# Kernel tuning notes

Hardware: AMD Instinct MI355X
Metric: run time of the kernel (lower is better)

## Reference

```python
import jax, jax.numpy as jnp
import numpy as np

N, B, HID, NPG, DEG, N_HOPS = 102400, 512, 256, 200, 32, 2
E = N * DEG
LN_EPS = 1e-5


def setup_inputs() -> dict:
    key = jax.random.key(0)
    ks = jax.random.split(key, 8)
    h = jax.random.normal(ks[0], (N, HID), jnp.float32)
    g = jax.random.normal(ks[1], (B, HID), jnp.float32)
    # sorted node->graph assignment, 200 nodes per graph
    batch = jnp.repeat(jnp.arange(B, dtype=jnp.int32), NPG)
    # intra-graph random edges: graph id per edge + local endpoints
    gid = jax.random.randint(ks[2], (E,), 0, B, jnp.int32)
    s_loc = jax.random.randint(ks[3], (E,), 0, NPG, jnp.int32)
    d_loc = jax.random.randint(ks[4], (E,), 0, NPG, jnp.int32)
    edge_index = jnp.stack([gid * NPG + s_loc, gid * NPG + d_loc])  # [2, E]
    # head MLP params: Linear(HID,2HID) -> LayerNorm(2HID) -> ReLU -> Linear(2HID,1)
    W1 = jax.random.normal(ks[5], (HID, 2 * HID), jnp.float32) * (1.0 / np.sqrt(HID))
    b1 = jnp.zeros((2 * HID,), jnp.float32)
    ln_g = jnp.ones((2 * HID,), jnp.float32)
    ln_b = jnp.zeros((2 * HID,), jnp.float32)
    W2 = jax.random.normal(ks[6], (2 * HID, 1), jnp.float32) * (1.0 / np.sqrt(2 * HID))
    b2 = jnp.zeros((1,), jnp.float32)
    return {"h": h, "g": g, "batch": batch, "edge_index": edge_index,
            "W1": W1, "b1": b1, "ln_g": ln_g, "ln_b": ln_b, "W2": W2, "b2": b2}


def reference(h, g, batch, edge_index, W1, b1, ln_g, ln_b, W2, b2):
    n = h.shape[0]
    nb = g.shape[0]
    # repeat_interleave(g, bincount(batch)) == g[batch] for sorted batch
    x = h + g[batch]                                   # [N, HID]
    z = x @ W1 + b1                                    # [N, 2*HID]
    mu = jnp.mean(z, axis=-1, keepdims=True)
    var = jnp.var(z, axis=-1, keepdims=True)           # biased, as torch LayerNorm
    z = (z - mu) * jax.lax.rsqrt(var + LN_EPS) * ln_g + ln_b
    z = jax.nn.relu(z)
    logits = (z @ W2 + b2)[:, 0]                       # [N]
    # segment softmax over each graph
    m = jax.ops.segment_max(logits, batch, num_segments=nb)
    e = jnp.exp(logits - m[batch])
    s = jax.ops.segment_sum(e, batch, num_segments=nb)
    node_prob = e / s[batch]                           # [N]
    pmax = jax.ops.segment_max(node_prob, batch, num_segments=nb)
    cand = jnp.where(node_prob >= pmax[batch], jnp.arange(n, dtype=jnp.int32), n)
    seed = jax.ops.segment_min(cand, batch, num_segments=nb)   # [B] global node ids
    # k_hop_subgraph BFS (PyG flow='source_to_target': expand target -> source)
    src, dst = edge_index[0], edge_index[1]
    nm = jnp.zeros((n,), jnp.int32).at[seed].set(1)
    for _ in range(N_HOPS):
        nm = jnp.maximum(nm, jnp.zeros((n,), jnp.int32).at[src].max(nm[dst]))
    nmb = nm > 0
    edge_mask = nmb[src] & nmb[dst]                    # [E] kept-edge mask
    edge_weight = logits[src] + logits[dst]            # [E]
    em = edge_mask.astype(jnp.int32)
    node_mask = (jnp.zeros((n,), jnp.int32).at[src].max(em).at[dst].max(em)) > 0
    return node_prob, edge_weight, edge_mask, node_mask
```

## Files before the change

### kernel.cpp

```cpp
#include <hip/hip_runtime.h>
#include <hip/hip_bf16.h>

#define HID 256
#define HID2 512
#define NPG 200
#define LN_EPS 1e-5f

typedef float f32x4 __attribute__((ext_vector_type(4)));
typedef short s16x8 __attribute__((ext_vector_type(8)));
typedef unsigned short ushort_t;

__device__ __forceinline__ ushort_t f2bf_rne(float x) {
    union { float f; unsigned int u; } c; c.f = x;
    unsigned int u = c.u;
    return (ushort_t)((u + 0x7fffu + ((u >> 16) & 1u)) >> 16);
}
__device__ __forceinline__ float bf2f(ushort_t h) {
    union { unsigned int u; float f; } c; c.u = ((unsigned int)h) << 16;
    return c.f;
}

__global__ __launch_bounds__(256)
void w1_prep_kernel(const float* __restrict__ W1,
                    ushort_t* __restrict__ w1h, ushort_t* __restrict__ w1l)
{
    const int col = blockIdx.x;
    const int k   = threadIdx.x;
    const float v = W1[(size_t)k * HID2 + col];
    const ushort_t hi = f2bf_rne(v);
    const ushort_t lo = f2bf_rne(v - bf2f(hi));
    const int tile = col >> 4, lc = col & 15;
    const int kq = k >> 5, gq = (k >> 3) & 3, j = k & 7;
    const size_t idx = ((((size_t)tile << 3) + kq) * 64 + (gq << 4) + lc) * 8 + j;
    w1h[idx] = hi;
    w1l[idx] = lo;
}

__global__ __launch_bounds__(512, 4)
void mlp_logits_mfma(const float* __restrict__ h, const float* __restrict__ g,
                     const int* __restrict__ batch,
                     const ushort_t* __restrict__ w1h, const ushort_t* __restrict__ w1l,
                     const float* __restrict__ b1,
                     const float* __restrict__ lng, const float* __restrict__ lnb,
                     const float* __restrict__ W2, const float* __restrict__ b2,
                     float* __restrict__ logits)
{
    __shared__ ushort_t xsh[64 * 256];
    __shared__ ushort_t xsl[64 * 256];
    __shared__ float prm[4 * 512];
    __shared__ float redS1[8][64];
    __shared__ float redS2[8][64];
    __shared__ float redT[8][64];
    __shared__ float muv[64], rsv[64];

    const int tid  = threadIdx.x;
    const int row0 = blockIdx.x * 64;

    {
        const int c = tid;
        prm[c]        = b1[c];
        prm[512 + c]  = lng[c];
        prm[1024 + c] = lnb[c];
        prm[1536 + c] = W2[c];
    }

    #pragma unroll
    for (int i = 0; i < 4; ++i) {
        const int ci = tid + (i << 9);
        const int r  = ci >> 5;
        const int kc = (ci & 31) << 3;
        const int grow = row0 + r;
        const int gb   = batch[grow];
        const f32x4* hp = reinterpret_cast<const f32x4*>(h + (size_t)grow * HID + kc);
        const f32x4* gp = reinterpret_cast<const f32x4*>(g + (size_t)gb   * HID + kc);
        const f32x4 h0 = __builtin_nontemporal_load(hp);
        const f32x4 h1 = __builtin_nontemporal_load(hp + 1);
        const f32x4 g0 = gp[0], g1 = gp[1];
        float xv[8] = { h0.x + g0.x, h0.y + g0.y, h0.z + g0.z, h0.w + g0.w,
                        h1.x + g1.x, h1.y + g1.y, h1.z + g1.z, h1.w + g1.w };
        ushort_t hh[8], ll[8];
        #pragma unroll
        for (int j = 0; j < 8; ++j) {
            const ushort_t hi = f2bf_rne(xv[j]);
            hh[j] = hi;
            ll[j] = f2bf_rne(xv[j] - bf2f(hi));
        }
        int byte_off = r * 512 + (kc << 1);
        byte_off ^= (r & 7) << 4;
        *reinterpret_cast<s16x8*>(reinterpret_cast<char*>(xsh) + byte_off) =
            *reinterpret_cast<const s16x8*>(hh);
        *reinterpret_cast<s16x8*>(reinterpret_cast<char*>(xsl) + byte_off) =
            *reinterpret_cast<const s16x8*>(ll);
    }
    __syncthreads();

    const int w  = tid >> 6;
    const int l  = tid & 63;
    const int lc = l & 15;
    const int gq = l >> 4;
    const int wcol0 = w << 6;

    f32x4 acc[4][4];
    #pragma unroll
    for (int rt = 0; rt < 4; ++rt)
        #pragma unroll
        for (int ct = 0; ct < 4; ++ct) acc[rt][ct] = (f32x4){0.f, 0.f, 0.f, 0.f};

    const ushort_t* bfh = w1h + (((size_t)w << 2) << 3) * 512 + (size_t)l * 8;
    const ushort_t* bfl = w1l + (((size_t)w << 2) << 3) * 512 + (size_t)l * 8;

    #pragma unroll
    for (int kq = 0; kq < 8; ++kq) {
        s16x8 bh[4], bl[4];
        #pragma unroll
        for (int ct = 0; ct < 4; ++ct) {
            const size_t foff = (size_t)((ct << 3) + kq) * 512;
            bh[ct] = *reinterpret_cast<const s16x8*>(bfh + foff);
            bl[ct] = *reinterpret_cast<const s16x8*>(bfl + foff);
        }
        s16x8 ah[4], al[4];
        #pragma unroll
        for (int rt = 0; rt < 4; ++rt) {
            const int arow = (rt << 4) | lc;
            int abyte = arow * 512 + (((kq << 5) + (gq << 3)) << 1);
            abyte ^= (arow & 7) << 4;
            ah[rt] = *reinterpret_cast<const s16x8*>(
                         reinterpret_cast<const char*>(xsh) + abyte);
            al[rt] = *reinterpret_cast<const s16x8*>(
                         reinterpret_cast<const char*>(xsl) + abyte);
        }
        #pragma unroll
        for (int ct = 0; ct < 4; ++ct)
            #pragma unroll
            for (int rt = 0; rt < 4; ++rt)
                acc[rt][ct] = __builtin_amdgcn_mfma_f32_16x16x32_bf16(ah[rt], bh[ct], acc[rt][ct], 0, 0, 0);
        #pragma unroll
        for (int ct = 0; ct < 4; ++ct)
            #pragma unroll
            for (int rt = 0; rt < 4; ++rt)
                acc[rt][ct] = __builtin_amdgcn_mfma_f32_16x16x32_bf16(al[rt], bh[ct], acc[rt][ct], 0, 0, 0);
        #pragma unroll
        for (int ct = 0; ct < 4; ++ct)
            #pragma unroll
            for (int rt = 0; rt < 4; ++rt)
                acc[rt][ct] = __builtin_amdgcn_mfma_f32_16x16x32_bf16(ah[rt], bl[ct], acc[rt][ct], 0, 0, 0);
    }

    #pragma unroll
    for (int rt = 0; rt < 4; ++rt) {
        float s1[4] = {0.f, 0.f, 0.f, 0.f};
        float s2[4] = {0.f, 0.f, 0.f, 0.f};
        #pragma unroll
        for (int ct = 0; ct < 4; ++ct) {
            const float bb = prm[wcol0 + (ct << 4) + lc];
            #pragma unroll
            for (int reg = 0; reg < 4; ++reg) {
                const float v = acc[rt][ct][reg] + bb;
                acc[rt][ct][reg] = v;
                s1[reg] += v;
                s2[reg] = fmaf(v, v, s2[reg]);
            }
        }
        #pragma unroll
        for (int reg = 0; reg < 4; ++reg) {
            float a = s1[reg], q = s2[reg];
            a += __shfl_xor(a, 1); q += __shfl_xor(q, 1);
            a += __shfl_xor(a, 2); q += __shfl_xor(q, 2);
            a += __shfl_xor(a, 4); q += __shfl_xor(q, 4);
            a += __shfl_xor(a, 8); q += __shfl_xor(q, 8);
            if (lc == 0) {
                const int row = (rt << 4) + (gq << 2) + reg;
                redS1[w][row] = a;
                redS2[w][row] = q;
            }
        }
    }
    __syncthreads();

    if (tid < 64) {
        float S1 = 0.f, S2 = 0.f;
        #pragma unroll
        for (int i = 0; i < 8; ++i) { S1 += redS1[i][tid]; S2 += redS2[i][tid]; }
        const float mu = S1 * (1.0f / HID2);
        const float var = S2 * (1.0f / HID2) - mu * mu;
        muv[tid] = mu;
        rsv[tid] = rsqrtf(var + LN_EPS);
    }
    __syncthreads();

    #pragma unroll
    for (int rt = 0; rt < 4; ++rt) {
        float tpart[4] = {0.f, 0.f, 0.f, 0.f};
        float mus[4], rss[4];
        #pragma unroll
        for (int reg = 0; reg < 4; ++reg) {
            const int row = (rt << 4) + (gq << 2) + reg;
            mus[reg] = muv[row];
            rss[reg] = rsv[row];
        }
        #pragma unroll
        for (int ct = 0; ct < 4; ++ct) {
            const int c = wcol0 + (ct << 4) + lc;
            const float lg = prm[512 + c], lb = prm[1024 + c], w2 = prm[1536 + c];
            #pragma unroll
            for (int reg = 0; reg < 4; ++reg) {
                float zn = (acc[rt][ct][reg] - mus[reg]) * rss[reg] * lg + lb;
                zn = fmaxf(zn, 0.f);
                tpart[reg] = fmaf(zn, w2, tpart[reg]);
            }
        }
        #pragma unroll
        for (int reg = 0; reg < 4; ++reg) {
            float t = tpart[reg];
            t += __shfl_xor(t, 1); t += __shfl_xor(t, 2);
            t += __shfl_xor(t, 4); t += __shfl_xor(t, 8);
            if (lc == 0) redT[w][(rt << 4) + (gq << 2) + reg] = t;
        }
    }
    __syncthreads();

    if (tid < 64) {
        float t = 0.f;
        #pragma unroll
        for (int i = 0; i < 8; ++i) t += redT[i][tid];
        logits[row0 + tid] = t + b2[0];
    }
}

__global__ __launch_bounds__(256)
void softmax_seed_kernel(const float* __restrict__ logits,
                         float* __restrict__ out_prob,
                         unsigned char* __restrict__ nm)
{
    const int gid  = blockIdx.x;
    const int tid  = threadIdx.x;
    const int node = gid * NPG + tid;
    const bool act = tid < NPG;

    __shared__ float redf[4];
    __shared__ int   redi[4];

    float l = act ? logits[node] : -INFINITY;

    float m = l;
    #pragma unroll
    for (int off = 32; off >= 1; off >>= 1) m = fmaxf(m, __shfl_xor(m, off));
    if ((tid & 63) == 0) redf[tid >> 6] = m;
    __syncthreads();
    const float bm = fmaxf(fmaxf(redf[0], redf[1]), fmaxf(redf[2], redf[3]));
    __syncthreads();

    const float e = act ? expf(l - bm) : 0.0f;
    float s = e;
    #pragma unroll
    for (int off = 32; off >= 1; off >>= 1) s += __shfl_xor(s, off);
    if ((tid & 63) == 0) redf[tid >> 6] = s;
    __syncthreads();
    const float bs = redf[0] + redf[1] + redf[2] + redf[3];
    __syncthreads();

    const float p = act ? e / bs : -1.0f;
    if (act) out_prob[node] = p;

    float pm = p;
    #pragma unroll
    for (int off = 32; off >= 1; off >>= 1) pm = fmaxf(pm, __shfl_xor(pm, off));
    if ((tid & 63) == 0) redf[tid >> 6] = pm;
    __syncthreads();
    const float bpm = fmaxf(fmaxf(redf[0], redf[1]), fmaxf(redf[2], redf[3]));

    int c = (act && p >= bpm) ? node : 0x7FFFFFFF;
    #pragma unroll
    for (int off = 32; off >= 1; off >>= 1) c = min(c, __shfl_xor(c, off));
    if ((tid & 63) == 0) redi[tid >> 6] = c;
    __syncthreads();
    if (tid == 0) {
        const int seed = min(min(redi[0], redi[1]), min(redi[2], redi[3]));
        nm[seed] = 1;
    }
}

__global__ __launch_bounds__(256)
void bfs_pass_kernel(const int* __restrict__ ei, unsigned char* __restrict__ nm,
                     const int E, const int maxlvl, const int newlvl)
{
    const int stride = gridDim.x * blockDim.x;
    for (int e = blockIdx.x * blockDim.x + threadIdx.x; e < E; e += stride) {
        const int d  = ei[E + e];
        const int lv = nm[d];
        if (lv >= 1 && lv <= maxlvl) {
            const int s = ei[e];
            if (nm[s] == 0) nm[s] = (unsigned char)newlvl;
        }
    }
}

__global__ __launch_bounds__(256)
void edge_out_kernel(const int* __restrict__ ei, const float* __restrict__ logits,
                     const unsigned char* __restrict__ nm,
                     float* __restrict__ out_ew,
                     float* __restrict__ out_em,
                     unsigned char* __restrict__ nodemask, const int E)
{
    const int e = (blockIdx.x * blockDim.x + threadIdx.x) << 2;
    if (e >= E) return;
    const int4 s4 = *reinterpret_cast<const int4*>(ei + e);
    const int4 d4 = *reinterpret_cast<const int4*>(ei + E + e);
    f32x4 ew, em;
    #pragma unroll
    for (int j = 0; j < 4; ++j) {
        const int s = (j == 0) ? s4.x : (j == 1) ? s4.y : (j == 2) ? s4.z : s4.w;
        const int d = (j == 0) ? d4.x : (j == 1) ? d4.y : (j == 2) ? d4.z : d4.w;
        ew[j] = logits[s] + logits[d];
        const bool m = (nm[s] != 0) && (nm[d] != 0);
        em[j] = m ? 1.0f : 0.0f;
        if (m) { nodemask[s] = 1; nodemask[d] = 1; }
    }
    *reinterpret_cast<f32x4*>(out_ew + e) = ew;
    *reinterpret_cast<f32x4*>(out_em + e) = em;
}

__global__ __launch_bounds__(256)
void node_mask_kernel(const unsigned char* __restrict__ nodemask,
                      float* __restrict__ out_nm, const int N)
{
    const int stride = gridDim.x * blockDim.x;
    for (int i = blockIdx.x * blockDim.x + threadIdx.x; i < N; i += stride)
        out_nm[i] = nodemask[i] ? 1.0f : 0.0f;
}

__global__ __launch_bounds__(256)
void zero_ws_kernel(uint4* __restrict__ p, const int n16)
{
    const int i = blockIdx.x * blockDim.x + threadIdx.x;
    if (i < n16) p[i] = make_uint4(0u, 0u, 0u, 0u);
}

extern "C" void kernel_launch(void* const* d_in, const int* in_sizes, int n_in,
                              void* d_out, int out_size, void* d_ws, size_t ws_size,
                              hipStream_t stream)
{
    const float* h     = (const float*)d_in[0];
    const float* g     = (const float*)d_in[1];
    const int*   batch = (const int*)d_in[2];
    const int*   ei    = (const int*)d_in[3];
    const float* W1    = (const float*)d_in[4];
    const float* b1    = (const float*)d_in[5];
    const float* lng   = (const float*)d_in[6];
    const float* lnb   = (const float*)d_in[7];
    const float* W2    = (const float*)d_in[8];
    const float* b2    = (const float*)d_in[9];

    const int N = in_sizes[2];
    const int E = in_sizes[3] / 2;

    float* out        = (float*)d_out;
    float* out_prob   = out;
    float* out_ew     = out + N;
    float* out_em     = out + (size_t)N + E;
    float* out_nmask  = out + (size_t)N + 2 * (size_t)E;

    char* ws = (char*)d_ws;
    float*         logits   = (float*)ws;
    ushort_t*      w1h      = (ushort_t*)(ws + (size_t)N * 4);
    ushort_t*      w1l      = (ushort_t*)(ws + (size_t)N * 4 + 262144);
    unsigned char* nm       = (unsigned char*)(ws + (size_t)N * 4 + 524288);
    unsigned char* nodemask = nm + N;

    const int n16 = (2 * N) / 16;
    zero_ws_kernel<<<(n16 + 255) / 256, 256, 0, stream>>>((uint4*)nm, n16);

    w1_prep_kernel<<<HID2, HID, 0, stream>>>(W1, w1h, w1l);

    mlp_logits_mfma<<<N / 64, 512, 0, stream>>>(h, g, batch, w1h, w1l,
                                                b1, lng, lnb, W2, b2, logits);
    softmax_seed_kernel<<<N / NPG, 256, 0, stream>>>(logits, out_prob, nm);
    bfs_pass_kernel<<<4096, 256, 0, stream>>>(ei, nm, E, 1, 2);
    bfs_pass_kernel<<<4096, 256, 0, stream>>>(ei, nm, E, 2, 3);
    edge_out_kernel<<<(E / 4 + 255) / 256, 256, 0, stream>>>(ei, logits, nm,
                                                             out_ew, out_em,
                                                             nodemask, E);
    node_mask_kernel<<<512, 256, 0, stream>>>(nodemask, out_nmask, N);
}
```

Baseline: 236.3 us.

## Vectorize BFS and node-mask kernels, stagger MFMA k-order and set wave priority

The BFS pass kernels now load four edges per thread with int4 loads over a one-edge-per-thread grid, replacing the grid-stride scalar loop. The node-mask kernel likewise converts four bytes per thread with vectorized stores. In the MLP kernel each wave starts its k-loop at a different offset to spread LDS bank and cache access, and raises its scheduling priority around the MFMA block. The vectorized loads assume E and N are multiples of four, and the BFS kernel now reads the source index for every edge, not only for edges whose destination is in the frontier.

```diff
diff --git a/kernel.cpp b/kernel.cpp
--- a/kernel.cpp
+++ b/kernel.cpp
@@ -110,7 +110,8 @@
     const ushort_t* bfl = w1l + (((size_t)w << 2) << 3) * 512 + (size_t)l * 8;
 
     #pragma unroll
-    for (int kq = 0; kq < 8; ++kq) {
+    for (int i = 0; i < 8; ++i) {
+        const int kq = (w + i) & 7;
         s16x8 bh[4], bl[4];
         #pragma unroll
         for (int ct = 0; ct < 4; ++ct) {
@@ -129,6 +130,7 @@
             al[rt] = *reinterpret_cast<const s16x8*>(
                          reinterpret_cast<const char*>(xsl) + abyte);
         }
+        __builtin_amdgcn_s_setprio(1);
         #pragma unroll
         for (int ct = 0; ct < 4; ++ct)
             #pragma unroll
@@ -144,6 +146,7 @@
             #pragma unroll
             for (int rt = 0; rt < 4; ++rt)
                 acc[rt][ct] = __builtin_amdgcn_mfma_f32_16x16x32_bf16(ah[rt], bl[ct], acc[rt][ct], 0, 0, 0);
+        __builtin_amdgcn_s_setprio(0);
     }
 
     #pragma unroll
@@ -284,12 +287,16 @@
 void bfs_pass_kernel(const int* __restrict__ ei, unsigned char* __restrict__ nm,
                      const int E, const int maxlvl, const int newlvl)
 {
-    const int stride = gridDim.x * blockDim.x;
-    for (int e = blockIdx.x * blockDim.x + threadIdx.x; e < E; e += stride) {
-        const int d  = ei[E + e];
+    const int e = (blockIdx.x * blockDim.x + threadIdx.x) << 2;
+    if (e >= E) return;
+    const int4 s4 = *reinterpret_cast<const int4*>(ei + e);
+    const int4 d4 = *reinterpret_cast<const int4*>(ei + E + e);
+    #pragma unroll
+    for (int j = 0; j < 4; ++j) {
+        const int d = (j == 0) ? d4.x : (j == 1) ? d4.y : (j == 2) ? d4.z : d4.w;
         const int lv = nm[d];
         if (lv >= 1 && lv <= maxlvl) {
-            const int s = ei[e];
+            const int s = (j == 0) ? s4.x : (j == 1) ? s4.y : (j == 2) ? s4.z : s4.w;
             if (nm[s] == 0) nm[s] = (unsigned char)newlvl;
         }
     }
@@ -324,9 +331,15 @@
 void node_mask_kernel(const unsigned char* __restrict__ nodemask,
                       float* __restrict__ out_nm, const int N)
 {
-    const int stride = gridDim.x * blockDim.x;
-    for (int i = blockIdx.x * blockDim.x + threadIdx.x; i < N; i += stride)
-        out_nm[i] = nodemask[i] ? 1.0f : 0.0f;
+    const int i = (blockIdx.x * blockDim.x + threadIdx.x) << 2;
+    if (i >= N) return;
+    const uchar4 m4 = *reinterpret_cast<const uchar4*>(nodemask + i);
+    f32x4 o;
+    o[0] = m4.x ? 1.0f : 0.0f;
+    o[1] = m4.y ? 1.0f : 0.0f;
+    o[2] = m4.z ? 1.0f : 0.0f;
+    o[3] = m4.w ? 1.0f : 0.0f;
+    *reinterpret_cast<f32x4*>(out_nm + i) = o;
 }
 
 __global__ __launch_bounds__(256)
@@ -375,10 +388,10 @@
     mlp_logits_mfma<<<N / 64, 512, 0, stream>>>(h, g, batch, w1h, w1l,
                                                 b1, lng, lnb, W2, b2, logits);
     softmax_seed_kernel<<<N / NPG, 256, 0, stream>>>(logits, out_prob, nm);
-    bfs_pass_kernel<<<4096, 256, 0, stream>>>(ei, nm, E, 1, 2);
-    bfs_pass_kernel<<<4096, 256, 0, stream>>>(ei, nm, E, 2, 3);
+    bfs_pass_kernel<<<(E / 4 + 255) / 256, 256, 0, stream>>>(ei, nm, E, 1, 2);
+    bfs_pass_kernel<<<(E / 4 + 255) / 256, 256, 0, stream>>>(ei, nm, E, 2, 3);
     edge_out_kernel<<<(E / 4 + 255) / 256, 256, 0, stream>>>(ei, logits, nm,
                                                              out_ew, out_em,
                                                              nodemask, E);
-    node_mask_kernel<<<512, 256, 0, stream>>>(nodemask, out_nmask, N);
-}
+    node_mask_kernel<<<(N / 4 + 255) / 256, 256, 0, stream>>>(nodemask, out_nmask, N);
+}
```

New measurement: 278.1 us. +17.7%, slower.
